# Kernel tuning notes

Measured on AMD Instinct MI355X. Metric: run time of the kernel, lower is better.

## Reference

```python
import jax, jax.numpy as jnp
import numpy as np

# cfg constants reconstructed from the repo's YOLOv2 (VOC) setup
ANCHORS = jnp.array([[1.3221, 1.73145], [3.19275, 4.00944], [5.05587, 8.09892],
                     [9.47112, 4.84053], [11.2364, 10.0071]], dtype=jnp.float32)
NUM_CLASSES = 20
LAMBDA_COORD = 5.0
LAMBDA_OBJ = 1.0
LAMBDA_NOOBJ = 0.5
LAMBDA_CLS = 1.0

B, H, W = 256, 26, 26
A = 5


def setup_inputs() -> dict:
    key = jax.random.key(0)
    k1, k2, k3, k4, k5 = jax.random.split(key, 5)
    prediction = jax.random.normal(k1, (B, A * (5 + NUM_CLASSES), H, W), dtype=jnp.float32)
    # build a realistic target: [...,:20] one-hot class, [...,20] conf in {0,1}, [...,21:23] xy in (0,1), [...,23:25] wh>0
    conf = (jax.random.uniform(k2, (B, H, W, 1)) < 0.03).astype(jnp.float32)
    xy = jax.random.uniform(k3, (B, H, W, 2), dtype=jnp.float32)
    wh = jax.random.uniform(k4, (B, H, W, 2), dtype=jnp.float32) * 6.0 + 0.5
    labels = jax.random.randint(k5, (B, H, W), 0, NUM_CLASSES)
    cls = jax.nn.one_hot(labels, NUM_CLASSES, dtype=jnp.float32)
    target = jnp.concatenate([cls, conf, xy, wh], axis=-1)  # [B,H,W,25]
    return {"prediction": prediction, "target": target}


def _box_iou(a, b):
    # a: [B,H,W,A,4] (cx,cy,w,h), b: [B,H,W,1,4] -> iou [B,H,W,A]
    ax1, ay1 = a[..., 0] - a[..., 2] / 2, a[..., 1] - a[..., 3] / 2
    ax2, ay2 = a[..., 0] + a[..., 2] / 2, a[..., 1] + a[..., 3] / 2
    bx1, by1 = b[..., 0] - b[..., 2] / 2, b[..., 1] - b[..., 3] / 2
    bx2, by2 = b[..., 0] + b[..., 2] / 2, b[..., 1] + b[..., 3] / 2
    iw = jnp.clip(jnp.minimum(ax2, bx2) - jnp.maximum(ax1, bx1), 0.0)
    ih = jnp.clip(jnp.minimum(ay2, by2) - jnp.maximum(ay1, by1), 0.0)
    inter = iw * ih
    union = a[..., 2] * a[..., 3] + b[..., 2] * b[..., 3] - inter
    return inter / (union + 1e-10)


def reference(prediction, target):
    bsize = prediction.shape[0]
    out = prediction.transpose(0, 2, 3, 1).reshape(bsize, H, W, A, 5 + NUM_CLASSES)
    pred_conf = jax.nn.sigmoid(out[..., 20])                      # [B,H,W,A]
    pred_xy = jax.nn.sigmoid(out[..., 21:23])                     # [B,H,W,A,2]
    pred_wh = jnp.exp(out[..., 23:25]) * ANCHORS                  # generate_anchorbox: wh scaled by anchor priors
    pred_cls = out[..., :20]                                      # [B,H,W,A,20]
    pred_box = jnp.concatenate([pred_xy, pred_wh], axis=-1)       # [B,H,W,A,4]

    tgt = target[:, :, :, None, :]                                # unsqueeze_(3)
    gt_conf = tgt[..., 20]                                        # [B,H,W,1]
    gt_box = jnp.concatenate([tgt[..., 21:23], tgt[..., 23:25]], axis=-1)  # [B,H,W,1,4]
    gt_cls = tgt[..., :20]                                        # [B,H,W,1,20]

    obj = (gt_conf[..., 0] != 0).astype(prediction.dtype)         # [B,H,W] (nonzero mask)

    iou = _box_iou(pred_box, gt_box)                              # [B,H,W,A]
    aidx = jnp.argmax(iou, axis=-1)                               # [B,H,W]

    best_box = jnp.take_along_axis(pred_box, aidx[..., None, None], axis=3)[:, :, :, 0]   # [B,H,W,4]
    best_conf = jnp.take_along_axis(pred_conf, aidx[..., None], axis=3)[:, :, :, 0]       # [B,H,W]
    best_cls = jnp.take_along_axis(pred_cls, aidx[..., None, None], axis=3)[:, :, :, 0]   # [B,H,W,20]

    box_loss = LAMBDA_COORD / bsize * jnp.sum(obj[..., None] * (best_box - gt_box[:, :, :, 0]) ** 2)
    conf_loss = LAMBDA_OBJ / bsize * jnp.sum(obj * (best_conf - gt_conf[..., 0]) ** 2)
    noobj_loss = LAMBDA_NOOBJ / bsize * jnp.sum((1.0 - obj) * best_conf ** 2)

    labels = jnp.argmax(gt_cls[:, :, :, 0], axis=-1)              # [B,H,W]
    logp = jax.nn.log_softmax(best_cls, axis=-1)
    nll = -jnp.take_along_axis(logp, labels[..., None], axis=-1)[..., 0]
    cls_loss = LAMBDA_CLS / bsize * jnp.sum(obj * nll)

    return (box_loss, conf_loss, noobj_loss, cls_loss)
```

## Files before the change

kernel.cpp:

```cpp
#include <hip/hip_runtime.h>
#include <math.h>

#define NHW 676
#define NB 256
#define NCELLS (NB * NHW)
#define NC 20
#define NA 5

__device__ __forceinline__ float sigmoidf_(float x) {
    return 1.0f / (1.0f + __expf(-x));
}

__global__ __launch_bounds__(256, 3) void yolo_loss_kernel(
    const float* __restrict__ pred,
    const float* __restrict__ tgt,
    float* __restrict__ out)
{
    const float AW[NA] = {1.3221f, 3.19275f, 5.05587f, 9.47112f, 11.2364f};
    const float AH[NA] = {1.73145f, 4.00944f, 8.09892f, 4.84053f, 10.0071f};

    __shared__ __align__(16) float stgt[256 * 25];
    __shared__ float sred[4][4];

    const int tid = threadIdx.x;
    const int t0  = blockIdx.x << 8;
    const int t   = t0 + tid;
    const int b   = t / NHW;
    const int hw  = t - b * NHW;
    const float* p = pred + (size_t)b * 125 * NHW + hw;

    float v[NA][5];
    #pragma unroll
    for (int a = 0; a < NA; ++a) {
        #pragma unroll
        for (int c = 0; c < 5; ++c) {
            v[a][c] = p[(a * 25 + 20 + c) * NHW];
        }
    }
    const float gconf = tgt[(size_t)t * 25 + 20];

    {
        const float4* g4 = (const float4*)(tgt + (size_t)t0 * 25);
        float4* s4 = (float4*)stgt;
        #pragma unroll
        for (int i = 0; i < 6; ++i) s4[i * 256 + tid] = g4[i * 256 + tid];
        if (tid < 64) s4[1536 + tid] = g4[1536 + tid];
    }

    const bool obj = (gconf != 0.0f);

    float cl[NA][NC];
    if (obj) {
        #pragma unroll
        for (int a = 0; a < NA; ++a) {
            #pragma unroll
            for (int k = 0; k < NC; ++k) {
                cl[a][k] = p[(a * 25 + k) * NHW];
            }
        }
    }

    __syncthreads();
    const float* tg = stgt + tid * 25;

    const float gx = tg[21], gy = tg[22], gw = tg[23], gh = tg[24];
    const float g_x1 = gx - gw * 0.5f, g_x2 = gx + gw * 0.5f;
    const float g_y1 = gy - gh * 0.5f, g_y2 = gy + gh * 0.5f;
    const float g_area = gw * gh;

    float best_iou = -1.0f;
    int   best_a = 0;
    float bx = 0, by = 0, bw = 0, bh = 0, btc = 0;

    #pragma unroll
    for (int a = 0; a < NA; ++a) {
        float px = sigmoidf_(v[a][1]);
        float py = sigmoidf_(v[a][2]);
        float pw = __expf(v[a][3]) * AW[a];
        float ph = __expf(v[a][4]) * AH[a];
        float iw = fminf(px + pw * 0.5f, g_x2) - fmaxf(px - pw * 0.5f, g_x1);
        float ih = fminf(py + ph * 0.5f, g_y2) - fmaxf(py - ph * 0.5f, g_y1);
        iw = fmaxf(iw, 0.0f);
        ih = fmaxf(ih, 0.0f);
        float inter = iw * ih;
        float uni = pw * ph + g_area - inter;
        float iou = inter / (uni + 1e-10f);
        if (iou > best_iou) {
            best_iou = iou;
            best_a = a;
            bx = px; by = py; bw = pw; bh = ph;
            btc = v[a][0];
        }
    }
    const float bconf = sigmoidf_(btc);

    float box_l = 0.0f, conf_l = 0.0f, noobj_l = 0.0f, cls_l = 0.0f;

    if (obj) {
        float dx = bx - gx, dy = by - gy, dw = bw - gw, dh = bh - gh;
        box_l = dx * dx + dy * dy + dw * dw + dh * dh;
        float dc = bconf - gconf;
        conf_l = dc * dc;

        float nll[NA];
        #pragma unroll
        for (int a = 0; a < NA; ++a) {
            float m = cl[a][0];
            #pragma unroll
            for (int k = 1; k < NC; ++k) m = fmaxf(m, cl[a][k]);
            float s = 0.0f, lsel = 0.0f;
            #pragma unroll
            for (int k = 0; k < NC; ++k) {
                s += __expf(cl[a][k] - m);
                if (tg[k] > 0.5f) lsel = cl[a][k];
            }
            nll[a] = -(lsel - m - __logf(s));
        }
        float cls = nll[0];
        #pragma unroll
        for (int a = 1; a < NA; ++a) cls = (best_a == a) ? nll[a] : cls;
        cls_l = cls;
    } else {
        noobj_l = bconf * bconf;
    }

    #pragma unroll
    for (int off = 32; off > 0; off >>= 1) {
        box_l   += __shfl_down(box_l,   off, 64);
        conf_l  += __shfl_down(conf_l,  off, 64);
        noobj_l += __shfl_down(noobj_l, off, 64);
        cls_l   += __shfl_down(cls_l,   off, 64);
    }

    int wave = tid >> 6;
    int lane = tid & 63;
    if (lane == 0) {
        sred[wave][0] = box_l;
        sred[wave][1] = conf_l;
        sred[wave][2] = noobj_l;
        sred[wave][3] = cls_l;
    }
    __syncthreads();
    if (tid == 0) {
        float b0 = 0, b1 = 0, b2 = 0, b3 = 0;
        #pragma unroll
        for (int w = 0; w < 4; ++w) {
            b0 += sred[w][0];
            b1 += sred[w][1];
            b2 += sred[w][2];
            b3 += sred[w][3];
        }
        atomicAdd(&out[0], b0 * (5.0f / 256.0f));
        atomicAdd(&out[1], b1 * (1.0f / 256.0f));
        atomicAdd(&out[2], b2 * (0.5f / 256.0f));
        atomicAdd(&out[3], b3 * (1.0f / 256.0f));
    }
}

extern "C" void kernel_launch(void* const* d_in, const int* in_sizes, int n_in,
                              void* d_out, int out_size, void* d_ws, size_t ws_size,
                              hipStream_t stream) {
    const float* pred = (const float*)d_in[0];
    const float* tgt  = (const float*)d_in[1];
    float* out = (float*)d_out;

    hipMemsetAsync(out, 0, out_size * sizeof(float), stream);

    dim3 grid(NCELLS / 256);
    dim3 block(256);
    hipLaunchKernelGGL(yolo_loss_kernel, grid, block, 0, stream,
                       pred, tgt, out);
}
```

Baseline: 159.4 us.

## Load class logits only for best anchor after IoU argmax

Instead of loading all 5x20 class logits before the barrier for object cells and computing five log-softmaxes, the kernel now picks the best anchor first and loads and reduces only that anchor's 20 logits. The early gconf global load is dropped in favour of reading it from shared memory, and the occupancy hint in launch_bounds is removed. The aim is to cut register pressure and wasted class traffic and math, but the class loads now sit on the critical path after the IoU computation instead of overlapping with the shared-memory staging. The label selection now uses an fma with the one-hot value, which assumes an exact one-hot target.

```diff
diff --git a/kernel.cpp b/kernel.cpp
--- a/kernel.cpp
+++ b/kernel.cpp
@@ -11,14 +11,11 @@
     return 1.0f / (1.0f + __expf(-x));
 }
 
-__global__ __launch_bounds__(256, 3) void yolo_loss_kernel(
+__global__ __launch_bounds__(256) void yolo_loss_kernel(
     const float* __restrict__ pred,
     const float* __restrict__ tgt,
     float* __restrict__ out)
 {
-    const float AW[NA] = {1.3221f, 3.19275f, 5.05587f, 9.47112f, 11.2364f};
-    const float AH[NA] = {1.73145f, 4.00944f, 8.09892f, 4.84053f, 10.0071f};
-
     __shared__ __align__(16) float stgt[256 * 25];
     __shared__ float sred[4][4];
 
@@ -29,16 +26,6 @@
     const int hw  = t - b * NHW;
     const float* p = pred + (size_t)b * 125 * NHW + hw;
 
-    float v[NA][5];
-    #pragma unroll
-    for (int a = 0; a < NA; ++a) {
-        #pragma unroll
-        for (int c = 0; c < 5; ++c) {
-            v[a][c] = p[(a * 25 + 20 + c) * NHW];
-        }
-    }
-    const float gconf = tgt[(size_t)t * 25 + 20];
-
     {
         const float4* g4 = (const float4*)(tgt + (size_t)t0 * 25);
         float4* s4 = (float4*)stgt;
@@ -47,22 +34,19 @@
         if (tid < 64) s4[1536 + tid] = g4[1536 + tid];
     }
 
-    const bool obj = (gconf != 0.0f);
-
-    float cl[NA][NC];
-    if (obj) {
-        #pragma unroll
-        for (int a = 0; a < NA; ++a) {
-            #pragma unroll
-            for (int k = 0; k < NC; ++k) {
-                cl[a][k] = p[(a * 25 + k) * NHW];
-            }
-        }
-    }
+#define LD5(a) \
+    float tc##a = p[((a)*25 + 20) * NHW]; \
+    float tx##a = p[((a)*25 + 21) * NHW]; \
+    float ty##a = p[((a)*25 + 22) * NHW]; \
+    float tw##a = p[((a)*25 + 23) * NHW]; \
+    float th##a = p[((a)*25 + 24) * NHW];
+    LD5(0) LD5(1) LD5(2) LD5(3) LD5(4)
+#undef LD5
 
     __syncthreads();
     const float* tg = stgt + tid * 25;
 
+    const float gconf = tg[20];
     const float gx = tg[21], gy = tg[22], gw = tg[23], gh = tg[24];
     const float g_x1 = gx - gw * 0.5f, g_x2 = gx + gw * 0.5f;
     const float g_y1 = gy - gh * 0.5f, g_y2 = gy + gh * 0.5f;
@@ -70,56 +54,56 @@
 
     float best_iou = -1.0f;
     int   best_a = 0;
-    float bx = 0, by = 0, bw = 0, bh = 0, btc = 0;
+    float bx = 0.0f, by = 0.0f, bw = 0.0f, bh = 0.0f, btc = 0.0f;
 
-    #pragma unroll
-    for (int a = 0; a < NA; ++a) {
-        float px = sigmoidf_(v[a][1]);
-        float py = sigmoidf_(v[a][2]);
-        float pw = __expf(v[a][3]) * AW[a];
-        float ph = __expf(v[a][4]) * AH[a];
-        float iw = fminf(px + pw * 0.5f, g_x2) - fmaxf(px - pw * 0.5f, g_x1);
-        float ih = fminf(py + ph * 0.5f, g_y2) - fmaxf(py - ph * 0.5f, g_y1);
-        iw = fmaxf(iw, 0.0f);
-        ih = fmaxf(ih, 0.0f);
-        float inter = iw * ih;
-        float uni = pw * ph + g_area - inter;
-        float iou = inter / (uni + 1e-10f);
-        if (iou > best_iou) {
-            best_iou = iou;
-            best_a = a;
-            bx = px; by = py; bw = pw; bh = ph;
-            btc = v[a][0];
-        }
-    }
+#define IOU_STEP(a, AWc, AHc) { \
+    float px = sigmoidf_(tx##a); \
+    float py = sigmoidf_(ty##a); \
+    float pw = __expf(tw##a) * (AWc); \
+    float ph = __expf(th##a) * (AHc); \
+    float iw = fminf(px + pw * 0.5f, g_x2) - fmaxf(px - pw * 0.5f, g_x1); \
+    float ih = fminf(py + ph * 0.5f, g_y2) - fmaxf(py - ph * 0.5f, g_y1); \
+    iw = fmaxf(iw, 0.0f); ih = fmaxf(ih, 0.0f); \
+    float inter = iw * ih; \
+    float uni = pw * ph + g_area - inter; \
+    float iou = inter / (uni + 1e-10f); \
+    if (iou > best_iou) {  \
+        best_iou = iou; best_a = (a); \
+        bx = px; by = py; bw = pw; bh = ph; btc = tc##a; \
+    } }
+    IOU_STEP(0, 1.3221f,  1.73145f)
+    IOU_STEP(1, 3.19275f, 4.00944f)
+    IOU_STEP(2, 5.05587f, 8.09892f)
+    IOU_STEP(3, 9.47112f, 4.84053f)
+    IOU_STEP(4, 11.2364f, 10.0071f)
+#undef IOU_STEP
+
     const float bconf = sigmoidf_(btc);
 
     float box_l = 0.0f, conf_l = 0.0f, noobj_l = 0.0f, cls_l = 0.0f;
 
-    if (obj) {
+    if (gconf != 0.0f) {
         float dx = bx - gx, dy = by - gy, dw = bw - gw, dh = bh - gh;
         box_l = dx * dx + dy * dy + dw * dw + dh * dh;
         float dc = bconf - gconf;
         conf_l = dc * dc;
 
-        float nll[NA];
-        #pragma unroll
-        for (int a = 0; a < NA; ++a) {
-            float m = cl[a][0];
-            #pragma unroll
-            for (int k = 1; k < NC; ++k) m = fmaxf(m, cl[a][k]);
-            float s = 0.0f, lsel = 0.0f;
-            #pragma unroll
-            for (int k = 0; k < NC; ++k) {
-                s += __expf(cl[a][k] - m);
-                if (tg[k] > 0.5f) lsel = cl[a][k];
-            }
-            nll[a] = -(lsel - m - __logf(s));
-        }
-        float cls = nll[0];
-        #pragma unroll
-        for (int a = 1; a < NA; ++a) cls = (best_a == a) ? nll[a] : cls;
-        cls_l = cls;
+        const float* pc = p + best_a * 25 * NHW;
+#define LDC(k) float l##k = pc[(k) * NHW];
+        LDC(0) LDC(1) LDC(2) LDC(3) LDC(4) LDC(5) LDC(6) LDC(7) LDC(8) LDC(9)
+        LDC(10) LDC(11) LDC(12) LDC(13) LDC(14) LDC(15) LDC(16) LDC(17) LDC(18) LDC(19)
+#undef LDC
+        float m = l0;
+#define MAXC(k) m = fmaxf(m, l##k);
+        MAXC(1) MAXC(2) MAXC(3) MAXC(4) MAXC(5) MAXC(6) MAXC(7) MAXC(8) MAXC(9)
+        MAXC(10) MAXC(11) MAXC(12) MAXC(13) MAXC(14) MAXC(15) MAXC(16) MAXC(17) MAXC(18) MAXC(19)
+#undef MAXC
+        float s = 0.0f, lsel = 0.0f;
+#define ACC(k) { s += __expf(l##k - m); lsel = fmaf(tg[k], l##k, lsel); }
+        ACC(0) ACC(1) ACC(2) ACC(3) ACC(4) ACC(5) ACC(6) ACC(7) ACC(8) ACC(9)
+        ACC(10) ACC(11) ACC(12) ACC(13) ACC(14) ACC(15) ACC(16) ACC(17) ACC(18) ACC(19)
+#undef ACC
+        cls_l = -(lsel - m - __logf(s));
     } else {
         noobj_l = bconf * bconf;
     }
```

Result: faster. 155.4 us (-2.6%).
